# Optimization experiments

Hardware: AMD Instinct MI355X
Metric: run time of the kernel (lower is better)

Reference implementation:

```python
import jax, jax.numpy as jnp
import numpy as np

N_HEADS = 16
N_KV_HEADS = 4
N_EMBED = 2048
HEAD_DIM = 128
SECTIONS = [16, 24, 24, 16, 24, 24]


def _process_rotary(c):
    # c: [3, B, T, HEAD_DIM] -> [B, 1, T, HEAD_DIM]
    splits = np.cumsum(SECTIONS)[:-1]
    secs = jnp.split(c, splits, axis=-1)
    out = jnp.concatenate([s[i % 3] for i, s in enumerate(secs)], axis=-1)
    return out[:, None]  # add head axis


def _rotate_half(x):
    x1, x2 = jnp.split(x, 2, axis=-1)
    return jnp.concatenate([-x2, x1], axis=-1)


def setup_inputs() -> dict:
    key = jax.random.key(0)
    ks = jax.random.split(key, 12)
    B, T = 1, 2048
    s = 0.02
    return {
        "x": jax.random.normal(ks[0], (B, T, N_EMBED), jnp.float32),
        "cos": jax.random.uniform(ks[1], (3, B, T, HEAD_DIM), jnp.float32),
        "sin": jax.random.uniform(ks[2], (3, B, T, HEAD_DIM), jnp.float32),
        "Wq": jax.random.normal(ks[3], (N_EMBED, N_EMBED), jnp.float32) * s,
        "bq": jax.random.normal(ks[4], (N_EMBED,), jnp.float32) * s,
        "Wk": jax.random.normal(ks[5], (N_EMBED, N_KV_HEADS * HEAD_DIM), jnp.float32) * s,
        "bk": jax.random.normal(ks[6], (N_KV_HEADS * HEAD_DIM,), jnp.float32) * s,
        "Wv": jax.random.normal(ks[7], (N_EMBED, N_KV_HEADS * HEAD_DIM), jnp.float32) * s,
        "bv": jax.random.normal(ks[8], (N_KV_HEADS * HEAD_DIM,), jnp.float32) * s,
        "Wo": jax.random.normal(ks[9], (N_EMBED, N_EMBED), jnp.float32) * s,
    }


def reference(x, cos, sin, Wq, bq, Wk, bk, Wv, bv, Wo):
    B, T, C = x.shape
    H, Hkv, D = N_HEADS, N_KV_HEADS, HEAD_DIM
    q = (x @ Wq + bq).reshape(B, T, H, D).transpose(0, 2, 1, 3)    # [B,H,T,D]
    k = (x @ Wk + bk).reshape(B, T, Hkv, D).transpose(0, 2, 1, 3)  # [B,Hkv,T,D]
    v = (x @ Wv + bv).reshape(B, T, Hkv, D).transpose(0, 2, 1, 3)
    # multi-section rope (cos/sin are 4-dim -> custom path)
    c = _process_rotary(cos)
    s = _process_rotary(sin)
    q = q * c + _rotate_half(q) * s
    k = k * c + _rotate_half(k) * s
    present_k, present_v = k, v
    # GQA expansion (repeat_interleave over head axis)
    r = H // Hkv
    k = jnp.repeat(k, r, axis=1)
    v = jnp.repeat(v, r, axis=1)
    # causal SDPA
    scores = jnp.einsum("bhqd,bhkd->bhqk", q, k) / jnp.sqrt(jnp.float32(D))
    causal = jnp.tril(jnp.ones((T, T), dtype=bool))
    scores = jnp.where(causal, scores, jnp.finfo(scores.dtype).min)
    attn = jax.nn.softmax(scores, axis=-1)
    y = jnp.einsum("bhqk,bhkd->bhqd", attn, v)
    y = y.transpose(0, 2, 1, 3).reshape(B, T, C)
    y = y @ Wo
    return (y, present_k, present_v)
```

## Files before the change

### kernel.cpp

```cpp
#include <hip/hip_runtime.h>

typedef unsigned short u16;
typedef __attribute__((ext_vector_type(4))) float f32x4;
typedef __attribute__((ext_vector_type(8))) __bf16 bf16x8;
typedef __attribute__((ext_vector_type(4))) u16 u16x4;


__device__ __forceinline__ u16 f2bf(float f) {
  union { float f; unsigned u; } v; v.f = f;
  unsigned r = v.u + 0x7fffu + ((v.u >> 16) & 1u);
  return (u16)(r >> 16);
}

__device__ __forceinline__ void stage16(const void* g, void* l) {
#if __has_builtin(__builtin_amdgcn_global_load_lds)
  __builtin_amdgcn_global_load_lds((const __attribute__((address_space(1))) void*)g,
                                   (__attribute__((address_space(3))) void*)l, 16, 0, 0);
#else
  *(f32x4*)l = *(const f32x4*)g;
#endif
}

__device__ __forceinline__ f32x4 mfma16(bf16x8 a, bf16x8 b, f32x4 c) {
  return __builtin_amdgcn_mfma_f32_16x16x32_bf16(a, b, c, 0, 0, 0);
}

__device__ __forceinline__ float fexp2(float x) {
#if __has_builtin(__builtin_amdgcn_exp2f)
  return __builtin_amdgcn_exp2f(x);
#else
  return exp2f(x);
#endif
}

__device__ __forceinline__ int rope_ch(int d) {
  int dd = (d < 64) ? d : d - 64;
  return (dd < 16) ? 0 : (dd < 40 ? 1 : 2);
}


__global__ void yuna_convert_bf16(const float* __restrict__ in, u16* __restrict__ out, int n4) {
  int i = blockIdx.x * blockDim.x + threadIdx.x;
  if (i < n4) {
    f32x4 v = ((const f32x4*)in)[i];
    u16x4 o;
    o.x = f2bf(v.x); o.y = f2bf(v.y); o.z = f2bf(v.z); o.w = f2bf(v.w);
    ((u16x4*)out)[i] = o;
  }
}

__global__ void yuna_prep_weights(const float* __restrict__ Wq, const float* __restrict__ Wk,
                                  const float* __restrict__ Wv, const float* __restrict__ Wo,
                                  u16* __restrict__ Wb, u16* __restrict__ Wob) {
  __shared__ float tile[64][65];
  const int mat = blockIdx.z;
  const float* W;
  u16* out;
  int N;
  if (mat == 0)      { W = Wq; out = Wb;                          N = 2048; }
  else if (mat == 1) { W = Wk; out = Wb + (size_t)2048 * 2048;    N = 512; }
  else if (mat == 2) { W = Wv; out = Wb + (size_t)2560 * 2048;    N = 512; }
  else               { W = Wo; out = Wob;                         N = 2048; }
  int k0 = blockIdx.x * 64, n0 = blockIdx.y * 64;
  if (n0 >= N) return;
  int tx = threadIdx.x & 63, ty = threadIdx.x >> 6;
#pragma unroll
  for (int j = 0; j < 64; j += 4)
    tile[ty + j][tx] = W[(size_t)(k0 + ty + j) * N + n0 + tx];
  __syncthreads();
#pragma unroll
  for (int j = 0; j < 64; j += 4)
    out[(size_t)(n0 + ty + j) * 2048 + k0 + tx] = f2bf(tile[tx][ty + j]);
}

__global__ void yuna_transpose_v(const float* __restrict__ pv, u16* __restrict__ vtb) {
  __shared__ float tile[64][65];
  int t0 = blockIdx.x * 64, d0 = blockIdx.y * 64, kvh = blockIdx.z;
  int tx = threadIdx.x & 63, ty = threadIdx.x >> 6;
#pragma unroll
  for (int j = 0; j < 64; j += 4)
    tile[ty + j][tx] = pv[(size_t)(kvh * 2048 + t0 + ty + j) * 128 + d0 + tx];
  __syncthreads();
#pragma unroll
  for (int j = 0; j < 64; j += 4)
    vtb[(size_t)(kvh * 128 + d0 + ty + j) * 2048 + t0 + tx] = f2bf(tile[tx][ty + j]);
}

template <int WN>
__global__ __launch_bounds__(256, 2) void yuna_gemm_bt(
    const u16* __restrict__ A, const u16* __restrict__ Bt,
    float* __restrict__ C, int M, int N, int K) {
  constexpr int NF = WN / 16;
  constexpr int BROWS = 2 * WN;
  __shared__ __align__(16) u16 As[128 * 64];
  __shared__ __align__(16) u16 Bs[BROWS * 64];
  const int tid = threadIdx.x;
  const int wave = tid >> 6, lane = tid & 63;
  const int m0 = blockIdx.x * 128, n0 = blockIdx.y * (2 * WN);
  const int wr = (wave >> 1) * 64, wc = (wave & 1) * WN;
  const int lrow = lane & 15, lkg = lane >> 4;

  const int srow = tid >> 3;
  const int ssc = (tid & 7) ^ ((tid >> 3) & 7);
  const size_t abase = (size_t)(m0 + srow) * K + ssc * 8;
  const size_t bbase = (size_t)(n0 + srow) * K + ssc * 8;

  const f32x4 fzero = {0.f, 0.f, 0.f, 0.f};
  f32x4 acc[4][NF];
#pragma unroll
  for (int mi = 0; mi < 4; ++mi)
#pragma unroll
    for (int ni = 0; ni < NF; ++ni) acc[mi][ni] = fzero;

  const int sw = lrow & 7;
  for (int k0 = 0; k0 < K; k0 += 64) {
    __syncthreads();
#pragma unroll
    for (int it = 0; it < 4; ++it)
      stage16(A + abase + (size_t)it * 32 * K + k0, (char*)As + (tid + it * 256) * 16);
#pragma unroll
    for (int it = 0; it < BROWS / 32; ++it)
      stage16(Bt + bbase + (size_t)it * 32 * K + k0, (char*)Bs + (tid + it * 256) * 16);
    asm volatile("s_waitcnt vmcnt(0)" ::: "memory");
    __syncthreads();
#pragma unroll
    for (int kk = 0; kk < 2; ++kk) {
      const int cof = ((kk * 4 + lkg) ^ sw) << 4;
      bf16x8 af[4], bfr[NF];
#pragma unroll
      for (int mi = 0; mi < 4; ++mi)
        af[mi] = *(const bf16x8*)((const char*)As + (wr + mi * 16 + lrow) * 128 + cof);
#pragma unroll
      for (int ni = 0; ni < NF; ++ni)
        bfr[ni] = *(const bf16x8*)((const char*)Bs + (wc + ni * 16 + lrow) * 128 + cof);
#pragma unroll
      for (int mi = 0; mi < 4; ++mi)
#pragma unroll
        for (int ni = 0; ni < NF; ++ni)
          acc[mi][ni] = mfma16(af[mi], bfr[ni], acc[mi][ni]);
    }
  }
#pragma unroll
  for (int mi = 0; mi < 4; ++mi)
#pragma unroll
    for (int ni = 0; ni < NF; ++ni) {
      int r0 = m0 + wr + mi * 16 + lkg * 4;
      int c = n0 + wc + ni * 16 + lrow;
#pragma unroll
      for (int r = 0; r < 4; ++r)
        C[(size_t)(r0 + r) * N + c] = acc[mi][ni][r];
    }
}

__global__ void yuna_rope_scatter(
    const float* __restrict__ qkv, const float* __restrict__ bq,
    const float* __restrict__ bk, const float* __restrict__ bv,
    const float* __restrict__ cosp, const float* __restrict__ sinp,
    u16* __restrict__ qb, u16* __restrict__ kb,
    float* __restrict__ pk, float* __restrict__ pv) {
  const float QSCALE = 1.4426950408889634f * 0.08838834764831845f;
  int t = blockIdx.x;
  int tid = threadIdx.x;
  const float* row = qkv + (size_t)t * 3072;
  size_t cbase = (size_t)t * 128;
  for (int i = tid; i < 1024; i += 256) {
    int h = i >> 6, d = i & 63;
    float a = row[h * 128 + d] + bq[h * 128 + d];
    float b = row[h * 128 + d + 64] + bq[h * 128 + d + 64];
    float c0 = cosp[(size_t)rope_ch(d) * 262144 + cbase + d];
    float s0 = sinp[(size_t)rope_ch(d) * 262144 + cbase + d];
    float c1 = cosp[(size_t)rope_ch(d + 64) * 262144 + cbase + d + 64];
    float s1 = sinp[(size_t)rope_ch(d + 64) * 262144 + cbase + d + 64];
    float o0 = a * c0 - b * s0;
    float o1 = b * c1 + a * s1;
    size_t o = ((size_t)h * 2048 + t) * 128 + d;
    qb[o] = f2bf(o0 * QSCALE);
    qb[o + 64] = f2bf(o1 * QSCALE);
  }
  {
    int kvh = tid >> 6, d = tid & 63;
    float a = row[2048 + kvh * 128 + d] + bk[kvh * 128 + d];
    float b = row[2048 + kvh * 128 + d + 64] + bk[kvh * 128 + d + 64];
    float c0 = cosp[(size_t)rope_ch(d) * 262144 + cbase + d];
    float s0 = sinp[(size_t)rope_ch(d) * 262144 + cbase + d];
    float c1 = cosp[(size_t)rope_ch(d + 64) * 262144 + cbase + d + 64];
    float s1 = sinp[(size_t)rope_ch(d + 64) * 262144 + cbase + d + 64];
    float o0 = a * c0 - b * s0;
    float o1 = b * c1 + a * s1;
    size_t o = ((size_t)kvh * 2048 + t) * 128 + d;
    kb[o] = f2bf(o0); kb[o + 64] = f2bf(o1);
    pk[o] = o0; pk[o + 64] = o1;
  }
  for (int i = tid; i < 512; i += 256) {
    int kvh = i >> 7, d = i & 127;
    pv[((size_t)kvh * 2048 + t) * 128 + d] = row[2560 + kvh * 128 + d] + bv[kvh * 128 + d];
  }
}

__global__ __launch_bounds__(128, 2) void yuna_flash_attn(
    const u16* __restrict__ Q,
    const u16* __restrict__ Kb,
    const u16* __restrict__ Vt,
    u16* __restrict__ Y) {
  __shared__ __align__(16) u16 Ks[2][64 * 128];
  __shared__ __align__(16) u16 Vs[2][128 * 64];
  __shared__ __align__(16) u16 Ps[64 * 64];
  const int h = blockIdx.x;
  const int yb = blockIdx.y;
  const int qb = (yb < 16) ? yb : 47 - yb;
  const int kvh = h >> 2;
  const int tid = threadIdx.x, wave = tid >> 6, lane = tid & 63;
  const int lrow = lane & 15, lkg = lane >> 4;
  const int mloc0 = wave * 32;
  const int sw = lrow & 7;

  const int krow = tid >> 4;
  const int ksc = (tid & 15) ^ ((tid >> 4) & 7);
  const size_t kbase0 = ((size_t)(kvh * 2048 + krow) << 7) + ksc * 8;
  const int vrow = tid >> 3;
  const int vsc = (tid & 7) ^ ((tid >> 3) & 7);
  const size_t vbase0 = (size_t)(kvh * 128 + vrow) * 2048 + vsc * 8;

  bf16x8 qf[2][4];
#pragma unroll
  for (int mt = 0; mt < 2; ++mt)
#pragma unroll
    for (int kk = 0; kk < 4; ++kk)
      qf[mt][kk] = *(const bf16x8*)(Q + (((size_t)h * 2048 + qb * 64 + mloc0 + mt * 16 + lrow) << 7) + kk * 32 + lkg * 8);

  const f32x4 fzero = {0.f, 0.f, 0.f, 0.f};
  f32x4 o[8][2];
#pragma unroll
  for (int dt = 0; dt < 8; ++dt) { o[dt][0] = fzero; o[dt][1] = fzero; }
  float m_i[2] = {-1e30f, -1e30f}, l_i[2] = {0.f, 0.f};

  const int nkb = qb + 1;

#pragma unroll
  for (int it = 0; it < 8; ++it)
    stage16(Kb + kbase0 + ((size_t)(it * 8) << 7), (char*)Ks[0] + (tid + it * 128) * 16);
#pragma unroll
  for (int it = 0; it < 8; ++it)
    stage16(Vt + vbase0 + (size_t)it * 16 * 2048, (char*)Vs[0] + (tid + it * 128) * 16);

  for (int kb = 0; kb < nkb; ++kb) {
    const int cur = kb & 1;
    const char* Ksb = (const char*)Ks[cur];
    const char* Vsb = (const char*)Vs[cur];
    if (kb + 1 < nkb) {
      char* Ksn = (char*)Ks[cur ^ 1];
      char* Vsn = (char*)Vs[cur ^ 1];
#pragma unroll
      for (int it = 0; it < 8; ++it)
        stage16(Kb + kbase0 + ((size_t)((kb + 1) * 64 + it * 8) << 7), Ksn + (tid + it * 128) * 16);
#pragma unroll
      for (int it = 0; it < 8; ++it)
        stage16(Vt + vbase0 + (size_t)it * 16 * 2048 + (kb + 1) * 64, Vsn + (tid + it * 128) * 16);
      asm volatile("s_waitcnt vmcnt(16)\n\ts_barrier" ::: "memory");
    } else {
      asm volatile("s_waitcnt vmcnt(0)\n\ts_barrier" ::: "memory");
    }

    f32x4 s[4][2];
#pragma unroll
    for (int nt = 0; nt < 4; ++nt) { s[nt][0] = fzero; s[nt][1] = fzero; }
#pragma unroll
    for (int kk = 0; kk < 4; ++kk) {
      const int cof = ((kk * 4 + lkg) ^ sw) << 4;
      bf16x8 kf[4];
#pragma unroll
      for (int nt = 0; nt < 4; ++nt)
        kf[nt] = *(const bf16x8*)(Ksb + (nt * 16 + lrow) * 256 + cof);
#pragma unroll
      for (int nt = 0; nt < 4; ++nt)
#pragma unroll
        for (int mt = 0; mt < 2; ++mt)
          s[nt][mt] = mfma16(kf[nt], qf[mt][kk], s[nt][mt]);
    }
    if (kb == qb) {
#pragma unroll
      for (int nt = 0; nt < 4; ++nt)
#pragma unroll
        for (int mt = 0; mt < 2; ++mt) {
          int m = mloc0 + mt * 16 + lrow;
#pragma unroll
          for (int r = 0; r < 4; ++r)
            if (nt * 16 + lkg * 4 + r > m) s[nt][mt][r] = -1e30f;
        }
    }

    float alpha[2];
#pragma unroll
    for (int mt = 0; mt < 2; ++mt) {
      float mx = -1e30f;
#pragma unroll
      for (int nt = 0; nt < 4; ++nt)
#pragma unroll
        for (int r = 0; r < 4; ++r) mx = fmaxf(mx, s[nt][mt][r]);
      mx = fmaxf(mx, __shfl_xor(mx, 16));
      mx = fmaxf(mx, __shfl_xor(mx, 32));
      float mnew = fmaxf(m_i[mt], mx);
      alpha[mt] = fexp2(m_i[mt] - mnew);
      m_i[mt] = mnew;
      float ps = 0.f;
      const int m = mloc0 + mt * 16 + lrow;
      const int hh = lkg & 1;
#pragma unroll
      for (int nt = 0; nt < 4; ++nt) {
        u16x4 p4;
#pragma unroll
        for (int r = 0; r < 4; ++r) {
          float p = fexp2(s[nt][mt][r] - mnew);
          ps += p;
          p4[r] = f2bf(p);
        }
        int cc = 2 * nt + (lkg >> 1);
        *(u16x4*)((char*)Ps + m * 128 + ((cc ^ (m & 7)) << 4) + hh * 8) = p4;
      }
      ps += __shfl_xor(ps, 16);
      ps += __shfl_xor(ps, 32);
      l_i[mt] = l_i[mt] * alpha[mt] + ps;
    }
#pragma unroll
    for (int dt = 0; dt < 8; ++dt) {
      o[dt][0] *= alpha[0];
      o[dt][1] *= alpha[1];
    }

#pragma unroll
    for (int kk = 0; kk < 2; ++kk) {
      const int cof = ((kk * 4 + lkg) ^ sw) << 4;
      bf16x8 pf[2], vf[8];
#pragma unroll
      for (int mt = 0; mt < 2; ++mt) {
        int m = mloc0 + mt * 16 + lrow;
        pf[mt] = *(const bf16x8*)((char*)Ps + m * 128 + cof);
      }
#pragma unroll
      for (int dt = 0; dt < 8; ++dt)
        vf[dt] = *(const bf16x8*)(Vsb + (dt * 16 + lrow) * 128 + cof);
#pragma unroll
      for (int dt = 0; dt < 8; ++dt)
#pragma unroll
        for (int mt = 0; mt < 2; ++mt)
          o[dt][mt] = mfma16(vf[dt], pf[mt], o[dt][mt]);
    }
    asm volatile("s_barrier" ::: "memory");
  }

  __syncthreads();
#pragma unroll
  for (int mt = 0; mt < 2; ++mt) {
    float inv = 1.f / l_i[mt];
    int m = mloc0 + mt * 16 + lrow;
    const int hh = lkg & 1;
#pragma unroll
    for (int dt = 0; dt < 8; ++dt) {
      u16x4 w4;
#pragma unroll
      for (int r = 0; r < 4; ++r) w4[r] = f2bf(o[dt][mt][r] * inv);
      int cc = 2 * dt + (lkg >> 1);
      *(u16x4*)((char*)Ks[0] + m * 256 + ((cc ^ (m & 7)) << 4) + hh * 8) = w4;
    }
  }
  __syncthreads();
#pragma unroll
  for (int it = 0; it < 8; ++it) {
    int c = tid + it * 128;
    int row = c >> 4, cc = c & 15;
    f32x4 v = *(const f32x4*)((const char*)Ks[0] + row * 256 + ((cc ^ (row & 7)) << 4));
    *(f32x4*)(Y + (size_t)(qb * 64 + row) * 2048 + h * 128 + cc * 8) = v;
  }
}


extern "C" void kernel_launch(void* const* d_in, const int* in_sizes, int n_in,
                              void* d_out, int out_size, void* d_ws, size_t ws_size,
                              hipStream_t stream) {
  const float* x = (const float*)d_in[0];
  const float* cosp = (const float*)d_in[1];
  const float* sinp = (const float*)d_in[2];
  const float* Wq = (const float*)d_in[3];
  const float* bq = (const float*)d_in[4];
  const float* Wk = (const float*)d_in[5];
  const float* bk = (const float*)d_in[6];
  const float* Wv = (const float*)d_in[7];
  const float* bv = (const float*)d_in[8];
  const float* Wo = (const float*)d_in[9];
  float* out = (float*)d_out;
  float* out_k = out + 4194304;
  float* out_v = out + 5242880;

  char* ws = (char*)d_ws;
  u16* xb   = (u16*)(ws + 0);
  u16* Wb   = (u16*)(ws + 8388608);
  u16* Wob  = (u16*)(ws + 20971520);
  float* qkv = (float*)(ws + 29360128);
  u16* qbuf = (u16*)(ws + 54525952);
  u16* kbuf = (u16*)(ws + 62914560);
  u16* vtb  = (u16*)(ws + 65011712);
  u16* yat  = (u16*)(ws + 67108864);

  yuna_convert_bf16<<<4096, 256, 0, stream>>>(x, xb, 1048576);
  yuna_prep_weights<<<dim3(32, 32, 4), 256, 0, stream>>>(Wq, Wk, Wv, Wo, Wb, Wob);
  yuna_gemm_bt<48><<<dim3(16, 32), 256, 0, stream>>>(xb, Wb, qkv, 2048, 3072, 2048);
  yuna_rope_scatter<<<2048, 256, 0, stream>>>(qkv, bq, bk, bv, cosp, sinp,
                                              qbuf, kbuf, out_k, out_v);
  yuna_transpose_v<<<dim3(32, 2, 4), 256, 0, stream>>>(out_v, vtb);
  yuna_flash_attn<<<dim3(16, 32), 128, 0, stream>>>(qbuf, kbuf, vtb, yat);
  yuna_gemm_bt<32><<<dim3(16, 32), 256, 0, stream>>>(yat, Wob, out, 2048, 2048, 2048);
}
```

Baseline: 267.7 us.

## Use four waves per attention block with one 16-row M tile each

The flash attention kernel moves from 2 waves each owning 32 query rows to 4 waves each owning 16 rows. K/V staging is split across 256 threads, and the vmcnt wait count is adjusted to match. Per-thread register state (Q fragments, O accumulators, scores) is halved, which should allow more waves per CU and better latency hiding. In exchange, each wave reuses its loaded K/V fragments across fewer MFMAs, so LDS read traffic per unit of compute rises. The bf16 conversion also switches to a perm-based pair packing that uses round-half-up instead of round-to-nearest-even.

```diff
diff --git a/kernel.cpp b/kernel.cpp
--- a/kernel.cpp
+++ b/kernel.cpp
@@ -1,15 +1,27 @@
 #include <hip/hip_runtime.h>
 
 typedef unsigned short u16;
+typedef unsigned int u32;
 typedef __attribute__((ext_vector_type(4))) float f32x4;
 typedef __attribute__((ext_vector_type(8))) __bf16 bf16x8;
 typedef __attribute__((ext_vector_type(4))) u16 u16x4;
+typedef __attribute__((ext_vector_type(2))) u32 u32x2;
 
 
 __device__ __forceinline__ u16 f2bf(float f) {
   union { float f; unsigned u; } v; v.f = f;
   unsigned r = v.u + 0x7fffu + ((v.u >> 16) & 1u);
   return (u16)(r >> 16);
+}
+
+__device__ __forceinline__ u32 pack_bf2(float a, float b) {
+  union { float f; unsigned u; } x, y;
+  x.f = a; y.f = b;
+#if __has_builtin(__builtin_amdgcn_perm)
+  return __builtin_amdgcn_perm(y.u + 0x8000u, x.u + 0x8000u, 0x07060302u);
+#else
+  return (u32)((x.u + 0x8000u) >> 16) | ((y.u + 0x8000u) & 0xffff0000u);
+#endif
 }
 
 __device__ __forceinline__ void stage16(const void* g, void* l) {
@@ -197,7 +209,7 @@
   }
 }
 
-__global__ __launch_bounds__(128, 2) void yuna_flash_attn(
+__global__ __launch_bounds__(256, 2) void yuna_flash_attn(
     const u16* __restrict__ Q,
     const u16* __restrict__ Kb,
     const u16* __restrict__ Vt,
@@ -211,7 +223,7 @@
   const int kvh = h >> 2;
   const int tid = threadIdx.x, wave = tid >> 6, lane = tid & 63;
   const int lrow = lane & 15, lkg = lane >> 4;
-  const int mloc0 = wave * 32;
+  const int m = wave * 16 + lrow;
   const int sw = lrow & 7;
 
   const int krow = tid >> 4;
@@ -221,27 +233,25 @@
   const int vsc = (tid & 7) ^ ((tid >> 3) & 7);
   const size_t vbase0 = (size_t)(kvh * 128 + vrow) * 2048 + vsc * 8;
 
-  bf16x8 qf[2][4];
-#pragma unroll
-  for (int mt = 0; mt < 2; ++mt)
-#pragma unroll
-    for (int kk = 0; kk < 4; ++kk)
-      qf[mt][kk] = *(const bf16x8*)(Q + (((size_t)h * 2048 + qb * 64 + mloc0 + mt * 16 + lrow) << 7) + kk * 32 + lkg * 8);
+  bf16x8 qf[4];
+#pragma unroll
+  for (int kk = 0; kk < 4; ++kk)
+    qf[kk] = *(const bf16x8*)(Q + (((size_t)h * 2048 + qb * 64 + m) << 7) + kk * 32 + lkg * 8);
 
   const f32x4 fzero = {0.f, 0.f, 0.f, 0.f};
-  f32x4 o[8][2];
-#pragma unroll
-  for (int dt = 0; dt < 8; ++dt) { o[dt][0] = fzero; o[dt][1] = fzero; }
-  float m_i[2] = {-1e30f, -1e30f}, l_i[2] = {0.f, 0.f};
+  f32x4 o[8];
+#pragma unroll
+  for (int dt = 0; dt < 8; ++dt) o[dt] = fzero;
+  float m_i = -1e30f, l_i = 0.f;
 
   const int nkb = qb + 1;
 
 #pragma unroll
-  for (int it = 0; it < 8; ++it)
-    stage16(Kb + kbase0 + ((size_t)(it * 8) << 7), (char*)Ks[0] + (tid + it * 128) * 16);
-#pragma unroll
-  for (int it = 0; it < 8; ++it)
-    stage16(Vt + vbase0 + (size_t)it * 16 * 2048, (char*)Vs[0] + (tid + it * 128) * 16);
+  for (int it = 0; it < 4; ++it)
+    stage16(Kb + kbase0 + ((size_t)(it * 16) << 7), (char*)Ks[0] + (tid + it * 256) * 16);
+#pragma unroll
+  for (int it = 0; it < 4; ++it)
+    stage16(Vt + vbase0 + (size_t)it * 32 * 2048, (char*)Vs[0] + (tid + it * 256) * 16);
 
   for (int kb = 0; kb < nkb; ++kb) {
     const int cur = kb & 1;
@@ -251,19 +261,19 @@
       char* Ksn = (char*)Ks[cur ^ 1];
       char* Vsn = (char*)Vs[cur ^ 1];
 #pragma unroll
-      for (int it = 0; it < 8; ++it)
-        stage16(Kb + kbase0 + ((size_t)((kb + 1) * 64 + it * 8) << 7), Ksn + (tid + it * 128) * 16);
-#pragma unroll
-      for (int it = 0; it < 8; ++it)
-        stage16(Vt + vbase0 + (size_t)it * 16 * 2048 + (kb + 1) * 64, Vsn + (tid + it * 128) * 16);
-      asm volatile("s_waitcnt vmcnt(16)\n\ts_barrier" ::: "memory");
+      for (int it = 0; it < 4; ++it)
+        stage16(Kb + kbase0 + ((size_t)((kb + 1) * 64 + it * 16) << 7), Ksn + (tid + it * 256) * 16);
+#pragma unroll
+      for (int it = 0; it < 4; ++it)
+        stage16(Vt + vbase0 + (size_t)it * 32 * 2048 + (kb + 1) * 64, Vsn + (tid + it * 256) * 16);
+      asm volatile("s_waitcnt vmcnt(8)\n\ts_barrier" ::: "memory");
     } else {
       asm volatile("s_waitcnt vmcnt(0)\n\ts_barrier" ::: "memory");
     }
 
-    f32x4 s[4][2];
-#pragma unroll
-    for (int nt = 0; nt < 4; ++nt) { s[nt][0] = fzero; s[nt][1] = fzero; }
+    f32x4 s[4];
+#pragma unroll
+    for (int nt = 0; nt < 4; ++nt) s[nt] = fzero;
 #pragma unroll
     for (int kk = 0; kk < 4; ++kk) {
       const int cof = ((kk * 4 + lkg) ^ sw) << 4;
@@ -273,100 +283,79 @@
         kf[nt] = *(const bf16x8*)(Ksb + (nt * 16 + lrow) * 256 + cof);
 #pragma unroll
       for (int nt = 0; nt < 4; ++nt)
-#pragma unroll
-        for (int mt = 0; mt < 2; ++mt)
-          s[nt][mt] = mfma16(kf[nt], qf[mt][kk], s[nt][mt]);
+        s[nt] = mfma16(kf[nt], qf[kk], s[nt]);
     }
     if (kb == qb) {
 #pragma unroll
       for (int nt = 0; nt < 4; ++nt)
 #pragma unroll
-        for (int mt = 0; mt < 2; ++mt) {
-          int m = mloc0 + mt * 16 + lrow;
-#pragma unroll
-          for (int r = 0; r < 4; ++r)
-            if (nt * 16 + lkg * 4 + r > m) s[nt][mt][r] = -1e30f;
-        }
-    }
-
-    float alpha[2];
-#pragma unroll
-    for (int mt = 0; mt < 2; ++mt) {
-      float mx = -1e30f;
-#pragma unroll
-      for (int nt = 0; nt < 4; ++nt)
-#pragma unroll
-        for (int r = 0; r < 4; ++r) mx = fmaxf(mx, s[nt][mt][r]);
-      mx = fmaxf(mx, __shfl_xor(mx, 16));
-      mx = fmaxf(mx, __shfl_xor(mx, 32));
-      float mnew = fmaxf(m_i[mt], mx);
-      alpha[mt] = fexp2(m_i[mt] - mnew);
-      m_i[mt] = mnew;
-      float ps = 0.f;
-      const int m = mloc0 + mt * 16 + lrow;
-      const int hh = lkg & 1;
-#pragma unroll
-      for (int nt = 0; nt < 4; ++nt) {
-        u16x4 p4;
-#pragma unroll
-        for (int r = 0; r < 4; ++r) {
-          float p = fexp2(s[nt][mt][r] - mnew);
-          ps += p;
-          p4[r] = f2bf(p);
-        }
-        int cc = 2 * nt + (lkg >> 1);
-        *(u16x4*)((char*)Ps + m * 128 + ((cc ^ (m & 7)) << 4) + hh * 8) = p4;
-      }
-      ps += __shfl_xor(ps, 16);
-      ps += __shfl_xor(ps, 32);
-      l_i[mt] = l_i[mt] * alpha[mt] + ps;
-    }
-#pragma unroll
-    for (int dt = 0; dt < 8; ++dt) {
-      o[dt][0] *= alpha[0];
-      o[dt][1] *= alpha[1];
-    }
+        for (int r = 0; r < 4; ++r)
+          if (nt * 16 + lkg * 4 + r > m) s[nt][r] = -1e30f;
+    }
+
+    float mx = -1e30f;
+#pragma unroll
+    for (int nt = 0; nt < 4; ++nt)
+#pragma unroll
+      for (int r = 0; r < 4; ++r) mx = fmaxf(mx, s[nt][r]);
+    mx = fmaxf(mx, __shfl_xor(mx, 16));
+    mx = fmaxf(mx, __shfl_xor(mx, 32));
+    float mnew = fmaxf(m_i, mx);
+    float alpha = fexp2(m_i - mnew);
+    m_i = mnew;
+    float ps = 0.f;
+    const int hh = lkg & 1;
+#pragma unroll
+    for (int nt = 0; nt < 4; ++nt) {
+      float p0 = fexp2(s[nt][0] - mnew);
+      float p1 = fexp2(s[nt][1] - mnew);
+      float p2 = fexp2(s[nt][2] - mnew);
+      float p3 = fexp2(s[nt][3] - mnew);
+      ps += (p0 + p1) + (p2 + p3);
+      u32x2 pk2;
+      pk2.x = pack_bf2(p0, p1);
+      pk2.y = pack_bf2(p2, p3);
+      int cc = 2 * nt + (lkg >> 1);
+      *(u32x2*)((char*)Ps + m * 128 + ((cc ^ (m & 7)) << 4) + hh * 8) = pk2;
+    }
+    ps += __shfl_xor(ps, 16);
+    ps += __shfl_xor(ps, 32);
+    l_i = l_i * alpha + ps;
+#pragma unroll
+    for (int dt = 0; dt < 8; ++dt) o[dt] *= alpha;
 
 #pragma unroll
     for (int kk = 0; kk < 2; ++kk) {
       const int cof = ((kk * 4 + lkg) ^ sw) << 4;
-      bf16x8 pf[2], vf[8];
-#pragma unroll
-      for (int mt = 0; mt < 2; ++mt) {
-        int m = mloc0 + mt * 16 + lrow;
-        pf[mt] = *(const bf16x8*)((char*)Ps + m * 128 + cof);
-      }
+      bf16x8 pf = *(const bf16x8*)((char*)Ps + m * 128 + cof);
+      bf16x8 vf[8];
 #pragma unroll
       for (int dt = 0; dt < 8; ++dt)
         vf[dt] = *(const bf16x8*)(Vsb + (dt * 16 + lrow) * 128 + cof);
 #pragma unroll
       for (int dt = 0; dt < 8; ++dt)
-#pragma unroll
-        for (int mt = 0; mt < 2; ++mt)
-          o[dt][mt] = mfma16(vf[dt], pf[mt], o[dt][mt]);
+        o[dt] = mfma16(vf[dt], pf, o[dt]);
     }
     asm volatile("s_barrier" ::: "memory");
   }
 
   __syncthreads();
-#pragma unroll
-  for (int mt = 0; mt < 2; ++mt) {
-    float inv = 1.f / l_i[mt];
-    int m = mloc0 + mt * 16 + lrow;
+  {
+    float inv = 1.f / l_i;
     const int hh = lkg & 1;
 #pragma unroll
     for (int dt = 0; dt < 8; ++dt) {
-      u16x4 w4;
-#pragma unroll
-      for (int r = 0; r < 4; ++r) w4[r] = f2bf(o[dt][mt][r] * inv);
+      u32x2 w2;
+      w2.x = pack_bf2(o[dt][0] * inv, o[dt][1] * inv);
+      w2.y = pack_bf2(o[dt][2] * inv, o[dt][3] * inv);
       int cc = 2 * dt + (lkg >> 1);
-      *(u16x4*)((char*)Ks[0] + m * 256 + ((cc ^ (m & 7)) << 4) + hh * 8) = w4;
+      *(u32x2*)((char*)Ks[0] + m * 256 + ((cc ^ (m & 7)) << 4) + hh * 8) = w2;
     }
   }
   __syncthreads();
 #pragma unroll
-  for (int it = 0; it < 8; ++it) {
-    int c = tid + it * 128;
+  for (int it = 0; it < 4; ++it) {
+    int c = tid + it * 256;
     int row = c >> 4, cc = c & 15;
     f32x4 v = *(const f32x4*)((const char*)Ks[0] + row * 256 + ((cc ^ (row & 7)) << 4));
     *(f32x4*)(Y + (size_t)(qb * 64 + row) * 2048 + h * 128 + cc * 8) = v;
@@ -407,6 +396,6 @@
   yuna_rope_scatter<<<2048, 256, 0, stream>>>(qkv, bq, bk, bv, cosp, sinp,
                                               qbuf, kbuf, out_k, out_v);
   yuna_transpose_v<<<dim3(32, 2, 4), 256, 0, stream>>>(out_v, vtb);
-  yuna_flash_attn<<<dim3(16, 32), 128, 0, stream>>>(qbuf, kbuf, vtb, yat);
+  yuna_flash_attn<<<dim3(16, 32), 256, 0, stream>>>(qbuf, kbuf, vtb, yat);
   yuna_gemm_bt<32><<<dim3(16, 32), 256, 0, stream>>>(yat, Wob, out, 2048, 2048, 2048);
 }
```

After: 242.2 us. 9.5% less time.
